# Kernel tuning notes

Measured on AMD Instinct MI355X. Metric: run time of the kernel, lower is better.

The kernel has to match this reference:

```python
import jax, jax.numpy as jnp
import numpy as np

N_GRAPHS = 64
NEG_SLOPE = 0.01  # default LeakyReLU slope
BN_EPS = 1e-5


def setup_inputs() -> dict:
    key = jax.random.key(0)
    ks = jax.random.split(key, 16)
    N, E, F_IN, H, H2, OUT, L = 50000, 800000, 64, 128, 64, 8, 3
    return {
        "x": jax.random.normal(ks[0], (N, F_IN), jnp.float32),
        "edge_index": jax.random.randint(ks[1], (2, E), 0, N, jnp.int32),
        "batch": jnp.sort(jax.random.randint(ks[2], (N,), 0, N_GRAPHS, jnp.int32)),
        "W_emb": jax.random.normal(ks[3], (F_IN, H), jnp.float32) * 0.05,
        "b_emb": jnp.zeros((H,), jnp.float32),
        "convW": jax.random.normal(ks[4], (L, H, H), jnp.float32) * 0.05,
        "convB": jnp.zeros((L, H), jnp.float32),
        "bn_gamma": jax.random.uniform(ks[5], (L, H), jnp.float32) + 0.5,
        "bn_beta": jax.random.normal(ks[6], (L, H), jnp.float32) * 0.1,
        "bn_mean": jax.random.normal(ks[7], (L, H), jnp.float32) * 0.1,
        "bn_var": jax.random.uniform(ks[8], (L, H), jnp.float32) + 0.5,
        "W1": jax.random.normal(ks[9], (H, H2), jnp.float32) * 0.05,
        "b1": jnp.zeros((H2,), jnp.float32),
        "W2": jax.random.normal(ks[10], (H2, OUT), jnp.float32) * 0.05,
        "b2": jnp.zeros((OUT,), jnp.float32),
    }


def reference(x, edge_index, batch, W_emb, b_emb, convW, convB,
              bn_gamma, bn_beta, bn_mean, bn_var, W1, b1, W2, b2):
    N = x.shape[0]
    # GCN normalization with self-loops (computed once; identical per layer)
    loop = jnp.arange(N, dtype=edge_index.dtype)
    s = jnp.concatenate([edge_index[0], loop])  # [E+N]
    d = jnp.concatenate([edge_index[1], loop])
    deg = jax.ops.segment_sum(jnp.ones(d.shape, x.dtype), d, num_segments=N)
    dinv = jax.lax.rsqrt(deg)  # deg >= 1 thanks to self-loops
    norm = dinv[s] * dinv[d]  # [E+N]

    h = x @ W_emb + b_emb  # node embedding, [N, H]
    L = convW.shape[0]
    for i in range(L):
        m = h @ convW[i]  # linear transform, [N, H]
        # gather-weight-scatter: sum_{(s->d)} norm * m[s]
        agg = jax.ops.segment_sum(m[s] * norm[:, None], d, num_segments=N) + convB[i]
        # BatchNorm (eval mode, running stats)
        hbn = (agg - bn_mean[i]) * jax.lax.rsqrt(bn_var[i] + BN_EPS) * bn_gamma[i] + bn_beta[i]
        h = jnp.where(hbn > 0, hbn, NEG_SLOPE * hbn)  # LeakyReLU
        # dropout is identity in eval mode

    g = jax.ops.segment_sum(h, batch, num_segments=N_GRAPHS)  # global_add_pool, [G, H]
    z = g @ W1 + b1
    z = jnp.where(z > 0, z, NEG_SLOPE * z)
    return z @ W2 + b2  # [G, OUT]
```

## Files before the change

### kernel.cpp

```cpp
#include <hip/hip_runtime.h>

#define NEG 0.01f
#define HF 128
#define BK 64
#define PB 512
#define SEG 40

typedef __attribute__((ext_vector_type(8))) short bf8;
typedef __attribute__((ext_vector_type(4))) float f4;
typedef __attribute__((ext_vector_type(2))) float f2;

__device__ __forceinline__ unsigned short f2bf(float v) {
    unsigned u = __float_as_uint(v);
    u = (u + 0x7fff + ((u >> 16) & 1)) >> 16;
    return (unsigned short)u;
}

__global__ __launch_bounds__(256) void k_mega1(
        const int* __restrict__ src, const int* __restrict__ dst, int E,
        int* __restrict__ cellcnt, int* __restrict__ binbuf,
        const float* __restrict__ x, const float* __restrict__ W_emb,
        const float* __restrict__ b_emb, short* __restrict__ hbuf, int N,
        const float* __restrict__ convW, short* __restrict__ wt_c, int L,
        const float* __restrict__ convB,
        const float* __restrict__ bn_g, const float* __restrict__ bn_b,
        const float* __restrict__ bn_m, const float* __restrict__ bn_v,
        float* __restrict__ scb, float* __restrict__ shb,
        int NBIN, int EB, int WB) {
    __shared__ short wt[128 * 88];
    __shared__ int lcur[256];
    const int bid = blockIdx.x;
    const int tid = threadIdx.x;

    if (bid < PB) {
        lcur[tid] = 0;
        __syncthreads();
        const int per = (E + PB - 1) / PB;
        const int e0 = bid * per;
        const int e1 = (e0 + per < E) ? e0 + per : E;
        for (int e = e0 + tid; e < e1; e += 256) {
            const int d = dst[e];
            const int b = d >> 8;
            const int p = atomicAdd(&lcur[b], 1);
            if (p < SEG)
                binbuf[((size_t)b * PB + bid) * SEG + p] = (src[e] << 8) | (d & 255);
        }
        __syncthreads();
        if (tid < NBIN) {
            int c = lcur[tid];
            cellcnt[(size_t)tid * PB + bid] = c < SEG ? c : SEG;
        }
        return;
    }
    if (bid < PB + EB) {
        for (int i = tid; i < 128 * 64; i += 256) {
            const int n = i >> 6, k = i & 63;
            wt[n * 88 + k] = (short)f2bf(W_emb[(size_t)k * HF + n]);
        }
        __syncthreads();
        const int wid = tid >> 6, lane = tid & 63;
        const int lr = lane & 15, lk = lane >> 4;
        const int m0 = (bid - PB) * 64 + wid * 16;
        if (m0 >= N) return;
        const int arow_i = m0 + lr < N ? m0 + lr : N - 1;
        bf8 a[2];
        const float* arow = x + (size_t)arow_i * 64 + lk * 8;
#pragma unroll
        for (int kk = 0; kk < 2; ++kk) {
            const float4 p = *reinterpret_cast<const float4*>(arow + kk * 32);
            const float4 q = *reinterpret_cast<const float4*>(arow + kk * 32 + 4);
            bf8 t;
            t[0] = (short)f2bf(p.x); t[1] = (short)f2bf(p.y);
            t[2] = (short)f2bf(p.z); t[3] = (short)f2bf(p.w);
            t[4] = (short)f2bf(q.x); t[5] = (short)f2bf(q.y);
            t[6] = (short)f2bf(q.z); t[7] = (short)f2bf(q.w);
            a[kk] = t;
        }
#pragma unroll
        for (int n = 0; n < 8; ++n) {
            f4 acc = {0.f, 0.f, 0.f, 0.f};
            const short* brow = wt + (n * 16 + lr) * 88 + lk * 8;
#pragma unroll
            for (int kk = 0; kk < 2; ++kk) {
                const bf8 b = *reinterpret_cast<const bf8*>(brow + kk * 32);
                acc = __builtin_amdgcn_mfma_f32_16x16x32_bf16(a[kk], b, acc, 0, 0, 0);
            }
            const int col = n * 16 + lr;
            const float bs = b_emb[col];
#pragma unroll
            for (int r = 0; r < 4; ++r)
                hbuf[(size_t)(m0 + lk * 4 + r) * HF + col] = (short)f2bf(acc[r] + bs);
        }
        return;
    }
    if (bid < PB + EB + WB) {
        const int i = (bid - PB - EB) * 256 + tid;
        const int per = HF * HF;
        if (i < L * per) {
            const int l = i / per, r = i % per;
            const int n = r / HF, k = r % HF;
            wt_c[i] = (short)f2bf(convW[(size_t)l * per + (size_t)k * HF + n]);
        }
        return;
    }
    const int i = (bid - PB - EB - WB) * 256 + tid;
    if (i < L * HF) {
        const float s = rsqrtf(bn_v[i] + 1e-5f) * bn_g[i];
        scb[i] = s;
        shb[i] = (convB[i] - bn_m[i]) * s + bn_b[i];
    }
}

__global__ __launch_bounds__(256) void k_binfill(
        const int* __restrict__ cellcnt, const int* __restrict__ binbuf,
        unsigned short* __restrict__ bkt, int* __restrict__ cnt,
        float* __restrict__ gbuf, short* __restrict__ mzero,
        int NBIN, int ZRIDX) {
    const int bid = blockIdx.x;
    const int tid = threadIdx.x;
    if (bid >= NBIN) {
        for (int i = tid; i < 64 * HF; i += 256) gbuf[i] = 0.0f;
        if (tid < 64) reinterpret_cast<int*>(mzero)[tid] = 0;
        return;
    }
    __shared__ int lcnt[256];
    lcnt[tid] = 0;
    __syncthreads();
    for (int sg = tid; sg < PB; sg += 256) {
        const int c = cellcnt[(size_t)bid * PB + sg];
        const int* segp = binbuf + ((size_t)bid * PB + sg) * SEG;
        for (int i = 0; i < c; ++i) {
            const int ed = segp[i];
            const int dl = ed & 255;
            const int p = atomicAdd(&lcnt[dl], 1);
            if (p < BK)
                bkt[(size_t)((bid << 8) + dl) * BK + p] =
                    (unsigned short)((unsigned)ed >> 8);
        }
    }
    __syncthreads();
    int c = lcnt[tid];
    if (c > BK) c = BK;
    const int pc = (c + 7) & ~7;
    const int node = (bid << 8) + tid;
    unsigned short* brow = bkt + (size_t)node * BK;
    for (int p = c; p < pc; ++p) brow[p] = (unsigned short)ZRIDX;
    cnt[node] = c;
}

__global__ __launch_bounds__(256) void k_gemm_conv(
        const short* __restrict__ A,
        const short* __restrict__ Bt,
        const int* __restrict__ cnt,
        short* __restrict__ C,
        int N) {
    const int tid = threadIdx.x;
    const int wid = tid >> 6, lane = tid & 63;
    const int lr = lane & 15, lk = lane >> 4;
    const int m0 = blockIdx.x * 128 + wid * 32;
    if (m0 >= N) return;
    bf8 aA[4], aB[4];
    const short* arowA = A + (size_t)(m0 + lr) * HF + lk * 8;
    const short* arowB = arowA + 16 * HF;
#pragma unroll
    for (int kk = 0; kk < 4; ++kk) {
        aA[kk] = *reinterpret_cast<const bf8*>(arowA + kk * 32);
        aB[kk] = *reinterpret_cast<const bf8*>(arowB + kk * 32);
    }
    float dvA[4], dvB[4];
#pragma unroll
    for (int r = 0; r < 4; ++r) {
        int rowA = m0 + lk * 4 + r;       if (rowA >= N) rowA = N - 1;
        int rowB = m0 + 16 + lk * 4 + r;  if (rowB >= N) rowB = N - 1;
        dvA[r] = rsqrtf((float)cnt[rowA] + 1.0f);
        dvB[r] = rsqrtf((float)cnt[rowB] + 1.0f);
    }
#pragma unroll
    for (int n = 0; n < 8; ++n) {
        f4 accA = {0.f, 0.f, 0.f, 0.f};
        f4 accB = {0.f, 0.f, 0.f, 0.f};
        const short* brow = Bt + (size_t)(n * 16 + lr) * HF + lk * 8;
#pragma unroll
        for (int kk = 0; kk < 4; ++kk) {
            const bf8 b = *reinterpret_cast<const bf8*>(brow + kk * 32);
            accA = __builtin_amdgcn_mfma_f32_16x16x32_bf16(aA[kk], b, accA, 0, 0, 0);
            accB = __builtin_amdgcn_mfma_f32_16x16x32_bf16(aB[kk], b, accB, 0, 0, 0);
        }
        const int col = n * 16 + lr;
#pragma unroll
        for (int r = 0; r < 4; ++r) {
            C[(size_t)(m0 + lk * 4 + r) * HF + col]      = (short)f2bf(accA[r] * dvA[r]);
            C[(size_t)(m0 + 16 + lk * 4 + r) * HF + col] = (short)f2bf(accB[r] * dvB[r]);
        }
    }
}

__global__ __launch_bounds__(256) void k_gather(
        const unsigned short* __restrict__ bkt, const int* __restrict__ cnt,
        const short* __restrict__ ms,
        const float* __restrict__ sc, const float* __restrict__ sh,
        short* __restrict__ h, int N) {
    const int wid  = (blockIdx.x * 256 + threadIdx.x) >> 6;
    const int lane = threadIdx.x & 63;
    const int sub  = lane >> 4;
    const int lf   = lane & 15;
    if (wid >= N) return;
    const size_t b0 = (size_t)wid * BK;
    const int myoff = ((int)bkt[b0 + lane]) << 8;
    const int deg = cnt[wid];
    const int pdeg = (deg + 7) & ~7;

    f2 acc[4];
#pragma unroll
    for (int j = 0; j < 4; ++j) acc[j] = (f2){0.f, 0.f};
    union U { bf8 v; unsigned u[4]; };

    U self;
    self.v = *reinterpret_cast<const bf8*>(ms + (size_t)wid * HF + lf * 8);

    const char* msb = (const char*)ms + lf * 16;
    for (int t = sub; t < pdeg; t += 8) {
        const int o0 = __shfl(myoff, t);
        const int o1 = __shfl(myoff, t + 4);
        U a, b;
        a.v = *reinterpret_cast<const bf8*>(msb + o0);
        b.v = *reinterpret_cast<const bf8*>(msb + o1);
#pragma unroll
        for (int j = 0; j < 4; ++j) {
            f2 va, vb;
            va.x = __uint_as_float(a.u[j] << 16);
            va.y = __uint_as_float(a.u[j] & 0xffff0000u);
            vb.x = __uint_as_float(b.u[j] << 16);
            vb.y = __uint_as_float(b.u[j] & 0xffff0000u);
            acc[j] += va + vb;
        }
    }
    if (sub == 0) {
#pragma unroll
        for (int j = 0; j < 4; ++j) {
            f2 val;
            val.x = __uint_as_float(self.u[j] << 16);
            val.y = __uint_as_float(self.u[j] & 0xffff0000u);
            acc[j] += val;
        }
    }
#pragma unroll
    for (int j = 0; j < 4; ++j) {
        acc[j].x += __shfl_xor(acc[j].x, 16);
        acc[j].y += __shfl_xor(acc[j].y, 16);
        acc[j].x += __shfl_xor(acc[j].x, 32);
        acc[j].y += __shfl_xor(acc[j].y, 32);
    }
    if (sub == 0) {
        const float dv = rsqrtf((float)deg + 1.0f);
        const int f0 = lf * 8;
        const float4 sca = *reinterpret_cast<const float4*>(sc + f0);
        const float4 scb2 = *reinterpret_cast<const float4*>(sc + f0 + 4);
        const float4 sha = *reinterpret_cast<const float4*>(sh + f0);
        const float4 shb2 = *reinterpret_cast<const float4*>(sh + f0 + 4);
        const float scv[8] = {sca.x, sca.y, sca.z, sca.w, scb2.x, scb2.y, scb2.z, scb2.w};
        const float shv[8] = {sha.x, sha.y, sha.z, sha.w, shb2.x, shb2.y, shb2.z, shb2.w};
        unsigned ou[4];
#pragma unroll
        for (int j = 0; j < 4; ++j) {
            float vx = fmaf(acc[j].x * dv, scv[2 * j],     shv[2 * j]);
            float vy = fmaf(acc[j].y * dv, scv[2 * j + 1], shv[2 * j + 1]);
            vx = fmaxf(vx, NEG * vx);
            vy = fmaxf(vy, NEG * vy);
            ou[j] = (unsigned)f2bf(vx) | ((unsigned)f2bf(vy) << 16);
        }
        *reinterpret_cast<uint4*>(h + (size_t)wid * HF + f0) =
            *reinterpret_cast<uint4*>(ou);
    }
}

__global__ __launch_bounds__(256) void k_pool(
        const short* __restrict__ h, const int* __restrict__ batch,
        float* __restrict__ g, int N, int per) {
    const int gwid = (blockIdx.x * 256 + threadIdx.x) >> 6;
    const int lane = threadIdx.x & 63;
    const int n0 = gwid * per;
    if (n0 >= N) return;
    const int n1 = (n0 + per < N) ? n0 + per : N;
    const int fp = lane * 2;
    float ax = 0.f, ay = 0.f;
    int cur = batch[n0];
    for (int n = n0; n < n1; ++n) {
        const int b = batch[n];
        if (b != cur) {
            atomicAdd(&g[cur * HF + fp], ax);
            atomicAdd(&g[cur * HF + fp + 1], ay);
            ax = 0.f; ay = 0.f; cur = b;
        }
        const unsigned u = *reinterpret_cast<const unsigned*>(h + (size_t)n * HF + fp);
        ax += __uint_as_float(u << 16);
        ay += __uint_as_float(u & 0xffff0000u);
    }
    atomicAdd(&g[cur * HF + fp], ax);
    atomicAdd(&g[cur * HF + fp + 1], ay);
}

__global__ __launch_bounds__(128) void k_mlp(
        const float* __restrict__ g, const float* __restrict__ W1,
        const float* __restrict__ b1, const float* __restrict__ W2,
        const float* __restrict__ b2, float* __restrict__ out) {
    __shared__ float gr[128];
    __shared__ float z[64];
    const int gid = blockIdx.x, t = threadIdx.x;
    gr[t] = g[gid * HF + t];
    __syncthreads();
    if (t < 64) {
        float acc = b1[t];
#pragma unroll 8
        for (int k = 0; k < 128; ++k) acc += gr[k] * W1[k * 64 + t];
        z[t] = acc > 0.0f ? acc : NEG * acc;
    }
    __syncthreads();
    if (t < 8) {
        float acc = b2[t];
#pragma unroll 8
        for (int j = 0; j < 64; ++j) acc += z[j] * W2[j * 8 + t];
        out[gid * 8 + t] = acc;
    }
}

extern "C" void kernel_launch(void* const* d_in, const int* in_sizes, int n_in,
                              void* d_out, int out_size, void* d_ws, size_t ws_size,
                              hipStream_t stream) {
    const float* x       = (const float*)d_in[0];
    const int*   eidx    = (const int*)  d_in[1];
    const int*   batch   = (const int*)  d_in[2];
    const float* W_emb   = (const float*)d_in[3];
    const float* b_emb   = (const float*)d_in[4];
    const float* convW   = (const float*)d_in[5];
    const float* convB   = (const float*)d_in[6];
    const float* bn_g    = (const float*)d_in[7];
    const float* bn_b    = (const float*)d_in[8];
    const float* bn_m    = (const float*)d_in[9];
    const float* bn_v    = (const float*)d_in[10];
    const float* W1      = (const float*)d_in[11];
    const float* b1      = (const float*)d_in[12];
    const float* W2      = (const float*)d_in[13];
    const float* b2      = (const float*)d_in[14];

    const int F_IN = 64;
    const int N = in_sizes[0] / F_IN;
    const int E = in_sizes[1] / 2;
    const int L = in_sizes[5] / (HF * HF);
    const int G = 64;

    const int* esrc = eidx;
    const int* edst = eidx + E;

    const int NBIN  = (N + 255) >> 8;
    const int Npad2 = NBIN << 8;
    const int Npad  = ((N + 127) / 128) * 128;

    unsigned short* bkt = (unsigned short*)d_ws;
    int* cnt      = (int*)(bkt + (size_t)Npad2 * BK);
    int* cellcnt  = cnt + Npad2;
    int* binbuf   = cellcnt + (size_t)NBIN * PB;
    short* hbuf   = (short*)(binbuf + (size_t)NBIN * PB * SEG);
    short* ms     = hbuf + (size_t)Npad * HF;
    short* wt_c   = ms + (size_t)(Npad + 128) * HF;
    float* gbuf   = (float*)(wt_c + (size_t)L * HF * HF);
    float* scb    = gbuf + G * HF;
    float* shb    = scb + L * HF;

    const int ZRIDX = Npad;

    const int EB = (N + 63) / 64;
    const int WB = (L * HF * HF + 255) / 256;
    const int SB = (L * HF + 255) / 256;
    k_mega1<<<PB + EB + WB + SB, 256, 0, stream>>>(
        esrc, edst, E, cellcnt, binbuf, x, W_emb, b_emb, hbuf, N,
        convW, wt_c, L, convB, bn_g, bn_b, bn_m, bn_v, scb, shb,
        NBIN, EB, WB);

    k_binfill<<<NBIN + 1, 256, 0, stream>>>(
        cellcnt, binbuf, bkt, cnt, gbuf, ms + (size_t)Npad * HF, NBIN, ZRIDX);

    for (int i = 0; i < L; ++i) {
        k_gemm_conv<<<(N + 127) / 128, 256, 0, stream>>>(
            hbuf, wt_c + (size_t)i * HF * HF, cnt, ms, N);
        k_gather<<<(N * 64 + 255) / 256, 256, 0, stream>>>(
            bkt, cnt, ms, scb + i * HF, shb + i * HF, hbuf, N);
    }

    const int nwaves = 256 * 4;
    const int per = (N + nwaves - 1) / nwaves;
    k_pool<<<256, 256, 0, stream>>>(hbuf, batch, gbuf, N, per);
    k_mlp<<<G, 128, 0, stream>>>(gbuf, W1, b1, W2, b2, (float*)d_out);
}
```

Before: 212.2 us.

## Fuse binfill, conv layers, pooling and MLP into one cooperative persistent kernel

Replaces the sequence of separate launches (bin fill, three GEMM+gather layer pairs, pool, MLP) with a single cooperative persistent kernel. Stages are separated by grid-wide barriers and each stage runs as a grid-stride loop. This is meant to remove per-launch overhead and the idle tails between roughly nine small kernels. In exchange it adds grid.sync costs, caps the grid at the occupancy-limited block count, and computes the grid size as maxb*256, which assumes 256 CUs.

```diff
diff --git a/kernel.cpp b/kernel.cpp
--- a/kernel.cpp
+++ b/kernel.cpp
@@ -1,4 +1,7 @@
 #include <hip/hip_runtime.h>
+#include <hip/hip_cooperative_groups.h>
+
+namespace cg = cooperative_groups;
 
 #define NEG 0.01f
 #define HF 128
@@ -111,216 +114,225 @@
     }
 }
 
-__global__ __launch_bounds__(256) void k_binfill(
+__global__ __launch_bounds__(256, 4) void k_fused(
         const int* __restrict__ cellcnt, const int* __restrict__ binbuf,
         unsigned short* __restrict__ bkt, int* __restrict__ cnt,
         float* __restrict__ gbuf, short* __restrict__ mzero,
-        int NBIN, int ZRIDX) {
-    const int bid = blockIdx.x;
-    const int tid = threadIdx.x;
-    if (bid >= NBIN) {
-        for (int i = tid; i < 64 * HF; i += 256) gbuf[i] = 0.0f;
-        if (tid < 64) reinterpret_cast<int*>(mzero)[tid] = 0;
-        return;
-    }
+        int NBIN, int ZRIDX,
+        short* __restrict__ hbuf, short* __restrict__ ms,
+        const short* __restrict__ wt_c,
+        const float* __restrict__ scb, const float* __restrict__ shb,
+        int L, int N,
+        const int* __restrict__ batch,
+        const float* __restrict__ W1, const float* __restrict__ b1,
+        const float* __restrict__ W2, const float* __restrict__ b2,
+        float* __restrict__ out) {
+    cg::grid_group grid = cg::this_grid();
     __shared__ int lcnt[256];
-    lcnt[tid] = 0;
-    __syncthreads();
-    for (int sg = tid; sg < PB; sg += 256) {
-        const int c = cellcnt[(size_t)bid * PB + sg];
-        const int* segp = binbuf + ((size_t)bid * PB + sg) * SEG;
-        for (int i = 0; i < c; ++i) {
-            const int ed = segp[i];
-            const int dl = ed & 255;
-            const int p = atomicAdd(&lcnt[dl], 1);
-            if (p < BK)
-                bkt[(size_t)((bid << 8) + dl) * BK + p] =
-                    (unsigned short)((unsigned)ed >> 8);
-        }
-    }
-    __syncthreads();
-    int c = lcnt[tid];
-    if (c > BK) c = BK;
-    const int pc = (c + 7) & ~7;
-    const int node = (bid << 8) + tid;
-    unsigned short* brow = bkt + (size_t)node * BK;
-    for (int p = c; p < pc; ++p) brow[p] = (unsigned short)ZRIDX;
-    cnt[node] = c;
-}
-
-__global__ __launch_bounds__(256) void k_gemm_conv(
-        const short* __restrict__ A,
-        const short* __restrict__ Bt,
-        const int* __restrict__ cnt,
-        short* __restrict__ C,
-        int N) {
-    const int tid = threadIdx.x;
-    const int wid = tid >> 6, lane = tid & 63;
-    const int lr = lane & 15, lk = lane >> 4;
-    const int m0 = blockIdx.x * 128 + wid * 32;
-    if (m0 >= N) return;
-    bf8 aA[4], aB[4];
-    const short* arowA = A + (size_t)(m0 + lr) * HF + lk * 8;
-    const short* arowB = arowA + 16 * HF;
-#pragma unroll
-    for (int kk = 0; kk < 4; ++kk) {
-        aA[kk] = *reinterpret_cast<const bf8*>(arowA + kk * 32);
-        aB[kk] = *reinterpret_cast<const bf8*>(arowB + kk * 32);
-    }
-    float dvA[4], dvB[4];
-#pragma unroll
-    for (int r = 0; r < 4; ++r) {
-        int rowA = m0 + lk * 4 + r;       if (rowA >= N) rowA = N - 1;
-        int rowB = m0 + 16 + lk * 4 + r;  if (rowB >= N) rowB = N - 1;
-        dvA[r] = rsqrtf((float)cnt[rowA] + 1.0f);
-        dvB[r] = rsqrtf((float)cnt[rowB] + 1.0f);
-    }
-#pragma unroll
-    for (int n = 0; n < 8; ++n) {
-        f4 accA = {0.f, 0.f, 0.f, 0.f};
-        f4 accB = {0.f, 0.f, 0.f, 0.f};
-        const short* brow = Bt + (size_t)(n * 16 + lr) * HF + lk * 8;
-#pragma unroll
-        for (int kk = 0; kk < 4; ++kk) {
-            const bf8 b = *reinterpret_cast<const bf8*>(brow + kk * 32);
-            accA = __builtin_amdgcn_mfma_f32_16x16x32_bf16(aA[kk], b, accA, 0, 0, 0);
-            accB = __builtin_amdgcn_mfma_f32_16x16x32_bf16(aB[kk], b, accB, 0, 0, 0);
-        }
-        const int col = n * 16 + lr;
-#pragma unroll
-        for (int r = 0; r < 4; ++r) {
-            C[(size_t)(m0 + lk * 4 + r) * HF + col]      = (short)f2bf(accA[r] * dvA[r]);
-            C[(size_t)(m0 + 16 + lk * 4 + r) * HF + col] = (short)f2bf(accB[r] * dvB[r]);
-        }
-    }
-}
-
-__global__ __launch_bounds__(256) void k_gather(
-        const unsigned short* __restrict__ bkt, const int* __restrict__ cnt,
-        const short* __restrict__ ms,
-        const float* __restrict__ sc, const float* __restrict__ sh,
-        short* __restrict__ h, int N) {
-    const int wid  = (blockIdx.x * 256 + threadIdx.x) >> 6;
-    const int lane = threadIdx.x & 63;
-    const int sub  = lane >> 4;
-    const int lf   = lane & 15;
-    if (wid >= N) return;
-    const size_t b0 = (size_t)wid * BK;
-    const int myoff = ((int)bkt[b0 + lane]) << 8;
-    const int deg = cnt[wid];
-    const int pdeg = (deg + 7) & ~7;
-
-    f2 acc[4];
-#pragma unroll
-    for (int j = 0; j < 4; ++j) acc[j] = (f2){0.f, 0.f};
-    union U { bf8 v; unsigned u[4]; };
-
-    U self;
-    self.v = *reinterpret_cast<const bf8*>(ms + (size_t)wid * HF + lf * 8);
-
-    const char* msb = (const char*)ms + lf * 16;
-    for (int t = sub; t < pdeg; t += 8) {
-        const int o0 = __shfl(myoff, t);
-        const int o1 = __shfl(myoff, t + 4);
-        U a, b;
-        a.v = *reinterpret_cast<const bf8*>(msb + o0);
-        b.v = *reinterpret_cast<const bf8*>(msb + o1);
-#pragma unroll
-        for (int j = 0; j < 4; ++j) {
-            f2 va, vb;
-            va.x = __uint_as_float(a.u[j] << 16);
-            va.y = __uint_as_float(a.u[j] & 0xffff0000u);
-            vb.x = __uint_as_float(b.u[j] << 16);
-            vb.y = __uint_as_float(b.u[j] & 0xffff0000u);
-            acc[j] += va + vb;
-        }
-    }
-    if (sub == 0) {
-#pragma unroll
-        for (int j = 0; j < 4; ++j) {
-            f2 val;
-            val.x = __uint_as_float(self.u[j] << 16);
-            val.y = __uint_as_float(self.u[j] & 0xffff0000u);
-            acc[j] += val;
-        }
-    }
-#pragma unroll
-    for (int j = 0; j < 4; ++j) {
-        acc[j].x += __shfl_xor(acc[j].x, 16);
-        acc[j].y += __shfl_xor(acc[j].y, 16);
-        acc[j].x += __shfl_xor(acc[j].x, 32);
-        acc[j].y += __shfl_xor(acc[j].y, 32);
-    }
-    if (sub == 0) {
-        const float dv = rsqrtf((float)deg + 1.0f);
-        const int f0 = lf * 8;
-        const float4 sca = *reinterpret_cast<const float4*>(sc + f0);
-        const float4 scb2 = *reinterpret_cast<const float4*>(sc + f0 + 4);
-        const float4 sha = *reinterpret_cast<const float4*>(sh + f0);
-        const float4 shb2 = *reinterpret_cast<const float4*>(sh + f0 + 4);
-        const float scv[8] = {sca.x, sca.y, sca.z, sca.w, scb2.x, scb2.y, scb2.z, scb2.w};
-        const float shv[8] = {sha.x, sha.y, sha.z, sha.w, shb2.x, shb2.y, shb2.z, shb2.w};
-        unsigned ou[4];
-#pragma unroll
-        for (int j = 0; j < 4; ++j) {
-            float vx = fmaf(acc[j].x * dv, scv[2 * j],     shv[2 * j]);
-            float vy = fmaf(acc[j].y * dv, scv[2 * j + 1], shv[2 * j + 1]);
-            vx = fmaxf(vx, NEG * vx);
-            vy = fmaxf(vy, NEG * vy);
-            ou[j] = (unsigned)f2bf(vx) | ((unsigned)f2bf(vy) << 16);
-        }
-        *reinterpret_cast<uint4*>(h + (size_t)wid * HF + f0) =
-            *reinterpret_cast<uint4*>(ou);
-    }
-}
-
-__global__ __launch_bounds__(256) void k_pool(
-        const short* __restrict__ h, const int* __restrict__ batch,
-        float* __restrict__ g, int N, int per) {
-    const int gwid = (blockIdx.x * 256 + threadIdx.x) >> 6;
-    const int lane = threadIdx.x & 63;
-    const int n0 = gwid * per;
-    if (n0 >= N) return;
-    const int n1 = (n0 + per < N) ? n0 + per : N;
-    const int fp = lane * 2;
-    float ax = 0.f, ay = 0.f;
-    int cur = batch[n0];
-    for (int n = n0; n < n1; ++n) {
-        const int b = batch[n];
-        if (b != cur) {
-            atomicAdd(&g[cur * HF + fp], ax);
-            atomicAdd(&g[cur * HF + fp + 1], ay);
-            ax = 0.f; ay = 0.f; cur = b;
-        }
-        const unsigned u = *reinterpret_cast<const unsigned*>(h + (size_t)n * HF + fp);
-        ax += __uint_as_float(u << 16);
-        ay += __uint_as_float(u & 0xffff0000u);
-    }
-    atomicAdd(&g[cur * HF + fp], ax);
-    atomicAdd(&g[cur * HF + fp + 1], ay);
-}
-
-__global__ __launch_bounds__(128) void k_mlp(
-        const float* __restrict__ g, const float* __restrict__ W1,
-        const float* __restrict__ b1, const float* __restrict__ W2,
-        const float* __restrict__ b2, float* __restrict__ out) {
     __shared__ float gr[128];
     __shared__ float z[64];
-    const int gid = blockIdx.x, t = threadIdx.x;
-    gr[t] = g[gid * HF + t];
-    __syncthreads();
-    if (t < 64) {
-        float acc = b1[t];
+    const int tid = threadIdx.x;
+    const int gdim = gridDim.x;
+    const int wid4 = tid >> 6, lane = tid & 63;
+
+    for (int bid = blockIdx.x; bid <= NBIN; bid += gdim) {
+        if (bid == NBIN) {
+            for (int i = tid; i < 64 * HF; i += 256) gbuf[i] = 0.0f;
+            if (tid < 64) reinterpret_cast<int*>(mzero)[tid] = 0;
+            continue;
+        }
+        lcnt[tid] = 0;
+        __syncthreads();
+        for (int sg = tid; sg < PB; sg += 256) {
+            const int c = cellcnt[(size_t)bid * PB + sg];
+            const int* segp = binbuf + ((size_t)bid * PB + sg) * SEG;
+            for (int i = 0; i < c; ++i) {
+                const int ed = segp[i];
+                const int dl = ed & 255;
+                const int p = atomicAdd(&lcnt[dl], 1);
+                if (p < BK)
+                    bkt[(size_t)((bid << 8) + dl) * BK + p] =
+                        (unsigned short)((unsigned)ed >> 8);
+            }
+        }
+        __syncthreads();
+        int c = lcnt[tid];
+        if (c > BK) c = BK;
+        const int pc = (c + 7) & ~7;
+        const int node = (bid << 8) + tid;
+        unsigned short* brow = bkt + (size_t)node * BK;
+        for (int p = c; p < pc; ++p) brow[p] = (unsigned short)ZRIDX;
+        cnt[node] = c;
+        __syncthreads();
+    }
+    grid.sync();
+
+    const int lr = lane & 15, lk = lane >> 4;
+    for (int l = 0; l < L; ++l) {
+        const short* Bt = wt_c + (size_t)l * HF * HF;
+        const int T = (N + 127) >> 7;
+        for (int bid = blockIdx.x; bid < T; bid += gdim) {
+            const int m0 = bid * 128 + wid4 * 32;
+            if (m0 >= N) continue;
+            bf8 aA[4], aB[4];
+            const short* arowA = hbuf + (size_t)(m0 + lr) * HF + lk * 8;
+            const short* arowB = arowA + 16 * HF;
+#pragma unroll
+            for (int kk = 0; kk < 4; ++kk) {
+                aA[kk] = *reinterpret_cast<const bf8*>(arowA + kk * 32);
+                aB[kk] = *reinterpret_cast<const bf8*>(arowB + kk * 32);
+            }
+            float dvA[4], dvB[4];
+#pragma unroll
+            for (int r = 0; r < 4; ++r) {
+                int rowA = m0 + lk * 4 + r;       if (rowA >= N) rowA = N - 1;
+                int rowB = m0 + 16 + lk * 4 + r;  if (rowB >= N) rowB = N - 1;
+                dvA[r] = rsqrtf((float)cnt[rowA] + 1.0f);
+                dvB[r] = rsqrtf((float)cnt[rowB] + 1.0f);
+            }
+#pragma unroll
+            for (int n = 0; n < 8; ++n) {
+                f4 accA = {0.f, 0.f, 0.f, 0.f};
+                f4 accB = {0.f, 0.f, 0.f, 0.f};
+                const short* brow = Bt + (size_t)(n * 16 + lr) * HF + lk * 8;
+#pragma unroll
+                for (int kk = 0; kk < 4; ++kk) {
+                    const bf8 b = *reinterpret_cast<const bf8*>(brow + kk * 32);
+                    accA = __builtin_amdgcn_mfma_f32_16x16x32_bf16(aA[kk], b, accA, 0, 0, 0);
+                    accB = __builtin_amdgcn_mfma_f32_16x16x32_bf16(aB[kk], b, accB, 0, 0, 0);
+                }
+                const int col = n * 16 + lr;
+#pragma unroll
+                for (int r = 0; r < 4; ++r) {
+                    ms[(size_t)(m0 + lk * 4 + r) * HF + col]      = (short)f2bf(accA[r] * dvA[r]);
+                    ms[(size_t)(m0 + 16 + lk * 4 + r) * HF + col] = (short)f2bf(accB[r] * dvB[r]);
+                }
+            }
+        }
+        grid.sync();
+
+        const float* sc = scb + l * HF;
+        const float* sh = shb + l * HF;
+        const int sub = lane >> 4;
+        const int lf  = lane & 15;
+        for (int base = blockIdx.x * 4; base < N; base += gdim * 4) {
+            const int node = base + wid4;
+            if (node >= N) continue;
+            const size_t b0 = (size_t)node * BK;
+            const int myoff = ((int)bkt[b0 + lane]) << 8;
+            const int deg = cnt[node];
+            const int pdeg = (deg + 7) & ~7;
+
+            f2 acc[4];
+#pragma unroll
+            for (int j = 0; j < 4; ++j) acc[j] = (f2){0.f, 0.f};
+            union U { bf8 v; unsigned u[4]; };
+
+            U self;
+            self.v = *reinterpret_cast<const bf8*>(ms + (size_t)node * HF + lf * 8);
+
+            const char* msb = (const char*)ms + lf * 16;
+            for (int t = sub; t < pdeg; t += 8) {
+                const int o0 = __shfl(myoff, t);
+                const int o1 = __shfl(myoff, t + 4);
+                U a, b;
+                a.v = *reinterpret_cast<const bf8*>(msb + o0);
+                b.v = *reinterpret_cast<const bf8*>(msb + o1);
+#pragma unroll
+                for (int j = 0; j < 4; ++j) {
+                    f2 va, vb;
+                    va.x = __uint_as_float(a.u[j] << 16);
+                    va.y = __uint_as_float(a.u[j] & 0xffff0000u);
+                    vb.x = __uint_as_float(b.u[j] << 16);
+                    vb.y = __uint_as_float(b.u[j] & 0xffff0000u);
+                    acc[j] += va + vb;
+                }
+            }
+            if (sub == 0) {
+#pragma unroll
+                for (int j = 0; j < 4; ++j) {
+                    f2 val;
+                    val.x = __uint_as_float(self.u[j] << 16);
+                    val.y = __uint_as_float(self.u[j] & 0xffff0000u);
+                    acc[j] += val;
+                }
+            }
+#pragma unroll
+            for (int j = 0; j < 4; ++j) {
+                acc[j].x += __shfl_xor(acc[j].x, 16);
+                acc[j].y += __shfl_xor(acc[j].y, 16);
+                acc[j].x += __shfl_xor(acc[j].x, 32);
+                acc[j].y += __shfl_xor(acc[j].y, 32);
+            }
+            if (sub == 0) {
+                const float dv = rsqrtf((float)deg + 1.0f);
+                const int f0 = lf * 8;
+                const float4 sca = *reinterpret_cast<const float4*>(sc + f0);
+                const float4 scb2 = *reinterpret_cast<const float4*>(sc + f0 + 4);
+                const float4 sha = *reinterpret_cast<const float4*>(sh + f0);
+                const float4 shb2 = *reinterpret_cast<const float4*>(sh + f0 + 4);
+                const float scv[8] = {sca.x, sca.y, sca.z, sca.w, scb2.x, scb2.y, scb2.z, scb2.w};
+                const float shv[8] = {sha.x, sha.y, sha.z, sha.w, shb2.x, shb2.y, shb2.z, shb2.w};
+                unsigned ou[4];
+#pragma unroll
+                for (int j = 0; j < 4; ++j) {
+                    float vx = fmaf(acc[j].x * dv, scv[2 * j],     shv[2 * j]);
+                    float vy = fmaf(acc[j].y * dv, scv[2 * j + 1], shv[2 * j + 1]);
+                    vx = fmaxf(vx, NEG * vx);
+                    vy = fmaxf(vy, NEG * vy);
+                    ou[j] = (unsigned)f2bf(vx) | ((unsigned)f2bf(vy) << 16);
+                }
+                *reinterpret_cast<uint4*>(hbuf + (size_t)node * HF + f0) =
+                    *reinterpret_cast<uint4*>(ou);
+            }
+        }
+        grid.sync();
+    }
+
+    {
+        const int totw = gdim * 4;
+        const int per = (N + totw - 1) / totw;
+        const int gwid = blockIdx.x * 4 + wid4;
+        const int n0 = gwid * per;
+        if (n0 < N) {
+            const int n1 = (n0 + per < N) ? n0 + per : N;
+            const int fp = lane * 2;
+            float ax = 0.f, ay = 0.f;
+            int cur = batch[n0];
+            for (int n = n0; n < n1; ++n) {
+                const int b = batch[n];
+                if (b != cur) {
+                    atomicAdd(&gbuf[cur * HF + fp], ax);
+                    atomicAdd(&gbuf[cur * HF + fp + 1], ay);
+                    ax = 0.f; ay = 0.f; cur = b;
+                }
+                const unsigned u = *reinterpret_cast<const unsigned*>(hbuf + (size_t)n * HF + fp);
+                ax += __uint_as_float(u << 16);
+                ay += __uint_as_float(u & 0xffff0000u);
+            }
+            atomicAdd(&gbuf[cur * HF + fp], ax);
+            atomicAdd(&gbuf[cur * HF + fp + 1], ay);
+        }
+    }
+    grid.sync();
+
+    if (blockIdx.x < 64) {
+        const int gid = blockIdx.x;
+        if (tid < 128) gr[tid] = gbuf[gid * HF + tid];
+        __syncthreads();
+        if (tid < 64) {
+            float acc = b1[tid];
 #pragma unroll 8
-        for (int k = 0; k < 128; ++k) acc += gr[k] * W1[k * 64 + t];
-        z[t] = acc > 0.0f ? acc : NEG * acc;
-    }
-    __syncthreads();
-    if (t < 8) {
-        float acc = b2[t];
+            for (int k = 0; k < 128; ++k) acc += gr[k] * W1[k * 64 + tid];
+            z[tid] = acc > 0.0f ? acc : NEG * acc;
+        }
+        __syncthreads();
+        if (tid < 8) {
+            float acc = b2[tid];
 #pragma unroll 8
-        for (int j = 0; j < 64; ++j) acc += z[j] * W2[j * 8 + t];
-        out[gid * 8 + t] = acc;
+            for (int j = 0; j < 64; ++j) acc += z[j] * W2[j * 8 + tid];
+            out[gid * 8 + tid] = acc;
+        }
     }
 }
 
@@ -366,8 +378,7 @@
     float* gbuf   = (float*)(wt_c + (size_t)L * HF * HF);
     float* scb    = gbuf + G * HF;
     float* shb    = scb + L * HF;
-
-    const int ZRIDX = Npad;
+    short* mzero  = ms + (size_t)Npad * HF;
 
     const int EB = (N + 63) / 64;
     const int WB = (L * HF * HF + 255) / 256;
@@ -377,18 +388,25 @@
         convW, wt_c, L, convB, bn_g, bn_b, bn_m, bn_v, scb, shb,
         NBIN, EB, WB);
 
-    k_binfill<<<NBIN + 1, 256, 0, stream>>>(
-        cellcnt, binbuf, bkt, cnt, gbuf, ms + (size_t)Npad * HF, NBIN, ZRIDX);
-
-    for (int i = 0; i < L; ++i) {
-        k_gemm_conv<<<(N + 127) / 128, 256, 0, stream>>>(
-            hbuf, wt_c + (size_t)i * HF * HF, cnt, ms, N);
-        k_gather<<<(N * 64 + 255) / 256, 256, 0, stream>>>(
-            bkt, cnt, ms, scb + i * HF, shb + i * HF, hbuf, N);
-    }
-
-    const int nwaves = 256 * 4;
-    const int per = (N + nwaves - 1) / nwaves;
-    k_pool<<<256, 256, 0, stream>>>(hbuf, batch, gbuf, N, per);
-    k_mlp<<<G, 128, 0, stream>>>(gbuf, W1, b1, W2, b2, (float*)d_out);
+    int gdim = 1024;
+    {
+        int maxb = 0;
+        if (hipOccupancyMaxActiveBlocksPerMultiprocessor(
+                &maxb, (const void*)k_fused, 256, 0) == hipSuccess && maxb > 0) {
+            const int cap = maxb * 256;
+            if (cap < gdim) gdim = cap;
+        } else {
+            gdim = 512;
+        }
+    }
+    int NBINv = NBIN, ZRIDXv = Npad, Lv = L, Nv = N;
+    float* outp = (float*)d_out;
+    void* kargs[] = {
+        (void*)&cellcnt, (void*)&binbuf, (void*)&bkt, (void*)&cnt,
+        (void*)&gbuf, (void*)&mzero, (void*)&NBINv, (void*)&ZRIDXv,
+        (void*)&hbuf, (void*)&ms, (void*)&wt_c,
+        (void*)&scb, (void*)&shb, (void*)&Lv, (void*)&Nv,
+        (void*)&batch, (void*)&W1, (void*)&b1, (void*)&W2, (void*)&b2,
+        (void*)&outp};
+    hipLaunchCooperativeKernel((void*)k_fused, dim3(gdim), dim3(256), kargs, 0, stream);
 }
```

Measured after the change: 756.2 us. 3.56x slower.
